# Kernel tuning notes

Hardware: AMD Instinct MI355X
Metric: run time of the kernel (lower is better)

Reference implementation:

```python
import jax, jax.numpy as jnp
import numpy as np

SCALE = 0.02  # init scale for weight matrices


def setup_inputs() -> dict:
    B, M, H = 2048, 64, 1024
    key = jax.random.key(0)
    ks = jax.random.split(key, 10)
    inp = {
        "pose_embed": jax.random.normal(ks[0], (B, H), jnp.float32),
        "query_embed": jax.random.normal(ks[1], (B, H), jnp.float32),
        "h": jax.random.normal(ks[2], (B, H), jnp.float32),
        "c": jax.random.normal(ks[3], (B, H), jnp.float32),
        "memory": jax.random.normal(ks[4], (B, M, H), jnp.float32),
        "W_ih": jax.random.normal(ks[5], (4 * H, H), jnp.float32) * SCALE,
        "W_hh": jax.random.normal(ks[6], (4 * H, H), jnp.float32) * SCALE,
        "b_ih": jnp.zeros((4 * H,), jnp.float32),
        "b_hh": jnp.zeros((4 * H,), jnp.float32),
        "Wq": jax.random.normal(ks[7], (H, H), jnp.float32) * SCALE,
        "bq": jnp.zeros((H,), jnp.float32),
        "Wk": jax.random.normal(ks[8], (H, H), jnp.float32) * SCALE,
        "bk": jnp.zeros((H,), jnp.float32),
        "Wv": jax.random.normal(ks[9], (H, H), jnp.float32) * SCALE,
        "bv": jnp.zeros((H,), jnp.float32),
    }
    return inp


def reference(pose_embed, query_embed, h, c, memory,
              W_ih, W_hh, b_ih, b_hh, Wq, bq, Wk, bk, Wv, bv):
    H = pose_embed.shape[-1]
    # --- LSTMCell step (torch gate order: i, f, g, o) ---
    gates = pose_embed @ W_ih.T + b_ih + h @ W_hh.T + b_hh  # [B, 4H]
    i_g, f_g, g_g, o_g = jnp.split(gates, 4, axis=-1)
    c_new = jax.nn.sigmoid(f_g) * c + jax.nn.sigmoid(i_g) * jnp.tanh(g_g)
    h_new = jax.nn.sigmoid(o_g) * jnp.tanh(c_new)
    # --- FIFO memory update (detach, pop oldest, append new h) ---
    mem = jnp.concatenate(
        [memory[:, 1:], jax.lax.stop_gradient(h_new)[:, None]], axis=1)  # [B, M, H]
    # --- single-query attention over memory ---
    Q = query_embed @ Wq.T + bq                       # [B, H]
    K = mem @ Wk.T + bk                               # [B, M, H]
    V = mem @ Wv.T + bv                               # [B, M, H]
    scores = jnp.einsum('bh,bmh->bm', Q, K) / jnp.sqrt(jnp.float32(H))
    attn = jax.nn.softmax(scores, axis=-1)            # [B, M]
    attended = jnp.einsum('bm,bmh->bh', attn, V)      # [B, H]
    return attended, h_new, c_new
```

## Files before the change

kernel.cpp:

```cpp
#include <hip/hip_runtime.h>
#include <stdint.h>

typedef __attribute__((ext_vector_type(8))) short short8;
typedef __attribute__((ext_vector_type(4))) float f32x4;
typedef unsigned short u16;

__device__ __forceinline__ u16 f2bf(float f) {
  union { float f; uint32_t u; } v; v.f = f;
  return (u16)((v.u + 0x7FFFu + ((v.u >> 16) & 1u)) >> 16);
}

__device__ __forceinline__ void gl_lds16(const void* g, void* l) {
  __builtin_amdgcn_global_load_lds(
      (const __attribute__((address_space(1))) void*)g,
      (__attribute__((address_space(3))) void*)l, 16, 0, 0);
}

__global__ __launch_bounds__(256) void gemm_bt(
    const u16* __restrict__ A, const u16* __restrict__ B,
    float* __restrict__ Cf, u16* __restrict__ Cb,
    const float* __restrict__ bias1,
    int M, int N, int K)
{
  __shared__ __align__(16) u16 As[128 * 32];
  __shared__ __align__(16) u16 Bs[128 * 32];
  const int t = threadIdx.x;
  const int lane = t & 63;
  const int w = t >> 6;
  const int wr = w >> 1, wc = w & 1;
  const int m0 = blockIdx.y * 128, n0 = blockIdx.x * 128;
  const int lr = lane & 15;
  const int lk = (lane >> 4) * 8;
  const int srow = t >> 2;
  const int scol = (t & 3) * 8;

  const u16* gA = A + (size_t)(m0 + srow) * K + scol;
  const u16* gB = B + (size_t)(n0 + srow) * K + scol;

  f32x4 acc[4][4] = {};

  for (int k0 = 0; k0 < K; k0 += 32) {
    gl_lds16(gA,                  As + t * 8);
    gl_lds16(gA + (size_t)64 * K, As + 2048 + t * 8);
    gl_lds16(gB,                  Bs + t * 8);
    gl_lds16(gB + (size_t)64 * K, Bs + 2048 + t * 8);
    gA += 32; gB += 32;
    __syncthreads();

    short8 a[4], b[4];
#pragma unroll
    for (int m = 0; m < 4; ++m)
      a[m] = *(const short8*)(As + (wr * 64 + m * 16 + lr) * 32 + lk);
#pragma unroll
    for (int n = 0; n < 4; ++n)
      b[n] = *(const short8*)(Bs + (wc * 64 + n * 16 + lr) * 32 + lk);
#pragma unroll
    for (int m = 0; m < 4; ++m)
#pragma unroll
      for (int n = 0; n < 4; ++n)
        acc[m][n] = __builtin_amdgcn_mfma_f32_16x16x32_bf16(a[m], b[n], acc[m][n], 0, 0, 0);
    __syncthreads();
  }

#pragma unroll
  for (int n = 0; n < 4; ++n) {
    int col = n0 + wc * 64 + n * 16 + lr;
    float bsum = bias1 ? bias1[col] : 0.f;
#pragma unroll
    for (int m = 0; m < 4; ++m) {
#pragma unroll
      for (int r = 0; r < 4; ++r) {
        int row = m0 + wr * 64 + m * 16 + (lane >> 4) * 4 + r;
        float vv = acc[m][n][r] + bsum;
        if (Cf) Cf[(size_t)row * N + col] = vv;
        if (Cb) Cb[(size_t)row * N + col] = f2bf(vv);
      }
    }
  }
}

__global__ __launch_bounds__(256) void prep_k(
    const float* __restrict__ pose, const float* __restrict__ h,
    const float* __restrict__ W_ih, const float* __restrict__ W_hh,
    const float* __restrict__ query, const float* __restrict__ Wv,
    const float* __restrict__ Wq, const float* __restrict__ Wk,
    u16* __restrict__ xcat, u16* __restrict__ wcat,
    u16* __restrict__ qry, u16* __restrict__ wvb,
    u16* __restrict__ wqb, u16* __restrict__ wktb)
{
  __shared__ u16 tile[64][65];
  int blk = blockIdx.x;
  int t = threadIdx.x;
  if (blk >= 16384) {
    int tblk = blk - 16384;
    int tr = (tblk >> 4) * 64, tc = (tblk & 15) * 64;
    int tx = t & 63;
    int ty = (t >> 6) * 16;
#pragma unroll
    for (int i = 0; i < 16; ++i)
      tile[ty + i][tx] = f2bf(Wk[(size_t)(tr + ty + i) * 1024 + tc + tx]);
    __syncthreads();
#pragma unroll
    for (int i = 0; i < 16; ++i)
      wktb[(size_t)(tc + ty + i) * 1024 + tr + tx] = tile[tx][ty + i];
    return;
  }
  const float* src; u16* dst; int ostride, ooff, base;
  if (blk < 2048)       { src = pose;  dst = xcat; ostride = 2048; ooff = 0;    base = 0; }
  else if (blk < 4096)  { src = h;     dst = xcat; ostride = 2048; ooff = 1024; base = 2048; }
  else if (blk < 8192)  { src = W_ih;  dst = wcat; ostride = 2048; ooff = 0;    base = 4096; }
  else if (blk < 12288) { src = W_hh;  dst = wcat; ostride = 2048; ooff = 1024; base = 8192; }
  else if (blk < 14336) { src = query; dst = qry;  ostride = 1024; ooff = 0;    base = 12288; }
  else if (blk < 15360) { src = Wv;    dst = wvb;  ostride = 1024; ooff = 0;    base = 14336; }
  else                  { src = Wq;    dst = wqb;  ostride = 1024; ooff = 0;    base = 15360; }
  int r = blk - base;
  int cc = t * 4;
  float4 v = *(const float4*)(src + (size_t)r * 1024 + cc);
  ushort4 o; o.x = f2bf(v.x); o.y = f2bf(v.y); o.z = f2bf(v.z); o.w = f2bf(v.w);
  *(ushort4*)(dst + (size_t)r * ostride + ooff + cc) = o;
}

__global__ __launch_bounds__(256, 3) void mega_k(
    const u16* __restrict__ Xcat, const u16* __restrict__ Wcat,
    float* __restrict__ gates,
    const float* __restrict__ b_ih, const float* __restrict__ b_hh,
    const float* __restrict__ Qk, const float* __restrict__ mem,
    float* __restrict__ attst)
{
  __shared__ __align__(16) u16 As[128 * 32];
  __shared__ __align__(16) u16 Bs[128 * 32];
  const int blk = blockIdx.x;
  const int t = threadIdx.x;
  const int lane = t & 63;

  if (blk % 3 != 2) {
    const int gid = (blk / 3) * 2 + (blk % 3);
    const int m0 = (gid >> 5) * 128, n0 = (gid & 31) * 128;
    const int w = t >> 6;
    const int wr = w >> 1, wc = w & 1;
    const int lr = lane & 15;
    const int lk = (lane >> 4) * 8;
    const int srow = t >> 2;
    const int scol = (t & 3) * 8;

    const u16* gA = Xcat + (size_t)(m0 + srow) * 2048 + scol;
    const u16* gB = Wcat + (size_t)(n0 + srow) * 2048 + scol;

    f32x4 acc[4][4] = {};
    for (int k0 = 0; k0 < 2048; k0 += 32) {
      gl_lds16(gA,                    As + t * 8);
      gl_lds16(gA + (size_t)64 * 2048, As + 2048 + t * 8);
      gl_lds16(gB,                    Bs + t * 8);
      gl_lds16(gB + (size_t)64 * 2048, Bs + 2048 + t * 8);
      gA += 32; gB += 32;
      __syncthreads();
      short8 a[4], b[4];
#pragma unroll
      for (int m = 0; m < 4; ++m)
        a[m] = *(const short8*)(As + (wr * 64 + m * 16 + lr) * 32 + lk);
#pragma unroll
      for (int n = 0; n < 4; ++n)
        b[n] = *(const short8*)(Bs + (wc * 64 + n * 16 + lr) * 32 + lk);
#pragma unroll
      for (int m = 0; m < 4; ++m)
#pragma unroll
        for (int n = 0; n < 4; ++n)
          acc[m][n] = __builtin_amdgcn_mfma_f32_16x16x32_bf16(a[m], b[n], acc[m][n], 0, 0, 0);
      __syncthreads();
    }
#pragma unroll
    for (int n = 0; n < 4; ++n) {
      int col = n0 + wc * 64 + n * 16 + lr;
      float bsum = b_ih[col] + b_hh[col];
#pragma unroll
      for (int m = 0; m < 4; ++m)
#pragma unroll
        for (int r = 0; r < 4; ++r) {
          int row = m0 + wr * 64 + m * 16 + (lane >> 4) * 4 + r;
          gates[(size_t)row * 4096 + col] = acc[m][n][r] + bsum;
        }
    }
  } else {
    const int ablk = blk / 3;
    const int wv_id = t >> 6;
    for (int bi = 0; bi < 2; ++bi) {
      const int b = ablk * 8 + wv_id * 2 + bi;
      const float* q = Qk + (size_t)b * 1024;
      float4 qv[4];
#pragma unroll
      for (int i = 0; i < 4; ++i)
        qv[i] = *(const float4*)(q + (i * 64 + lane) * 4);
      const float* mb = mem + (size_t)b * 65536;

      float m_run = -3e38f, l = 0.f;
      float4 cx[4] = {};

      for (int qd = 0; qd < 15; ++qd) {
        const float* r0 = mb + (size_t)(1 + qd * 4) * 1024;
        float4 rv[4][4];
        float s[4] = {0.f, 0.f, 0.f, 0.f};
#pragma unroll
        for (int rr = 0; rr < 4; ++rr)
#pragma unroll
          for (int i = 0; i < 4; ++i) {
            rv[rr][i] = *(const float4*)(r0 + rr * 1024 + (i * 64 + lane) * 4);
            s[rr] += rv[rr][i].x * qv[i].x + rv[rr][i].y * qv[i].y +
                     rv[rr][i].z * qv[i].z + rv[rr][i].w * qv[i].w;
          }
#pragma unroll
        for (int rr = 0; rr < 4; ++rr) {
#pragma unroll
          for (int off = 32; off; off >>= 1) s[rr] += __shfl_xor(s[rr], off);
          s[rr] *= 0.03125f;
        }
#pragma unroll
        for (int rr = 0; rr < 4; ++rr) {
          if (s[rr] <= m_run + 8.f) {
            float e = __expf(s[rr] - m_run);
            l += e;
#pragma unroll
            for (int i = 0; i < 4; ++i) {
              cx[i].x += e * rv[rr][i].x; cx[i].y += e * rv[rr][i].y;
              cx[i].z += e * rv[rr][i].z; cx[i].w += e * rv[rr][i].w;
            }
          } else {
            float sc = __expf(m_run - s[rr]);
            m_run = s[rr];
            l = l * sc + 1.f;
#pragma unroll
            for (int i = 0; i < 4; ++i) {
              cx[i].x = cx[i].x * sc + rv[rr][i].x; cx[i].y = cx[i].y * sc + rv[rr][i].y;
              cx[i].z = cx[i].z * sc + rv[rr][i].z; cx[i].w = cx[i].w * sc + rv[rr][i].w;
            }
          }
        }
      }
      for (int r = 61; r <= 63; ++r) {
        const float* row = mb + (size_t)r * 1024;
        float4 rv[4];
        float s = 0.f;
#pragma unroll
        for (int i = 0; i < 4; ++i) {
          rv[i] = *(const float4*)(row + (i * 64 + lane) * 4);
          s += rv[i].x * qv[i].x + rv[i].y * qv[i].y + rv[i].z * qv[i].z + rv[i].w * qv[i].w;
        }
#pragma unroll
        for (int off = 32; off; off >>= 1) s += __shfl_xor(s, off);
        s *= 0.03125f;
        if (s <= m_run + 8.f) {
          float e = __expf(s - m_run);
          l += e;
#pragma unroll
          for (int i = 0; i < 4; ++i) {
            cx[i].x += e * rv[i].x; cx[i].y += e * rv[i].y;
            cx[i].z += e * rv[i].z; cx[i].w += e * rv[i].w;
          }
        } else {
          float sc = __expf(m_run - s);
          m_run = s;
          l = l * sc + 1.f;
#pragma unroll
          for (int i = 0; i < 4; ++i) {
            cx[i].x = cx[i].x * sc + rv[i].x; cx[i].y = cx[i].y * sc + rv[i].y;
            cx[i].z = cx[i].z * sc + rv[i].z; cx[i].w = cx[i].w * sc + rv[i].w;
          }
        }
      }
      float* st = attst + (size_t)b * 1032;
#pragma unroll
      for (int i = 0; i < 4; ++i)
        *(float4*)(st + (i * 64 + lane) * 4) = cx[i];
      if (lane == 0) { st[1024] = m_run; st[1025] = l; }
    }
  }
}

__global__ __launch_bounds__(256) void lstmfin_k(
    const float* __restrict__ gates, const float* __restrict__ c,
    const float* __restrict__ Qk, const float* __restrict__ attst,
    float* __restrict__ out_h, float* __restrict__ out_c,
    u16* __restrict__ ctxb)
{
  const int b = blockIdx.x;
  const int t = threadIdx.x;
  const int lane = t & 63, wv_id = t >> 6;
  const int p = t * 4;
  const float* g = gates + (size_t)b * 4096;
  float4 ig = *(const float4*)(g + p);
  float4 fg = *(const float4*)(g + 1024 + p);
  float4 gg = *(const float4*)(g + 2048 + p);
  float4 og = *(const float4*)(g + 3072 + p);
  float4 cv = *(const float4*)(c + (size_t)b * 1024 + p);

  float hn[4], cn[4];
  {
    float igs[4] = {ig.x, ig.y, ig.z, ig.w};
    float fgs[4] = {fg.x, fg.y, fg.z, fg.w};
    float ggs[4] = {gg.x, gg.y, gg.z, gg.w};
    float ogs[4] = {og.x, og.y, og.z, og.w};
    float cvs[4] = {cv.x, cv.y, cv.z, cv.w};
#pragma unroll
    for (int j = 0; j < 4; ++j) {
      float si = 1.f / (1.f + __expf(-igs[j]));
      float sf = 1.f / (1.f + __expf(-fgs[j]));
      float so = 1.f / (1.f + __expf(-ogs[j]));
      float tg = 2.f / (1.f + __expf(-2.f * ggs[j])) - 1.f;
      cn[j] = sf * cvs[j] + si * tg;
      float tc2 = 2.f / (1.f + __expf(-2.f * cn[j])) - 1.f;
      hn[j] = so * tc2;
    }
  }
  *(float4*)(out_c + (size_t)b * 1024 + p) = make_float4(cn[0], cn[1], cn[2], cn[3]);
  *(float4*)(out_h + (size_t)b * 1024 + p) = make_float4(hn[0], hn[1], hn[2], hn[3]);

  float4 qv = *(const float4*)(Qk + (size_t)b * 1024 + p);
  float part = qv.x * hn[0] + qv.y * hn[1] + qv.z * hn[2] + qv.w * hn[3];
#pragma unroll
  for (int off = 32; off; off >>= 1) part += __shfl_xor(part, off);
  __shared__ float red[4];
  if (lane == 0) red[wv_id] = part;
  __syncthreads();
  float s_last = (red[0] + red[1] + red[2] + red[3]) * 0.03125f;

  const float* st = attst + (size_t)b * 1032;
  float m_run = st[1024], l = st[1025];
  float4 cx = *(const float4*)(st + p);
  if (s_last <= m_run + 8.f) {
    float e = __expf(s_last - m_run);
    l += e;
    cx.x += e * hn[0]; cx.y += e * hn[1]; cx.z += e * hn[2]; cx.w += e * hn[3];
  } else {
    float sc = __expf(m_run - s_last);
    l = l * sc + 1.f;
    cx.x = cx.x * sc + hn[0]; cx.y = cx.y * sc + hn[1];
    cx.z = cx.z * sc + hn[2]; cx.w = cx.w * sc + hn[3];
  }
  float inv = 1.f / l;
  ushort4 o;
  o.x = f2bf(cx.x * inv); o.y = f2bf(cx.y * inv);
  o.z = f2bf(cx.z * inv); o.w = f2bf(cx.w * inv);
  *(ushort4*)(ctxb + (size_t)b * 1024 + p) = o;
}

extern "C" void kernel_launch(void* const* d_in, const int* in_sizes, int n_in,
                              void* d_out, int out_size, void* d_ws, size_t ws_size,
                              hipStream_t stream) {
  const int Bb = 2048, Hh = 1024;
  const float* pose  = (const float*)d_in[0];
  const float* query = (const float*)d_in[1];
  const float* h     = (const float*)d_in[2];
  const float* c     = (const float*)d_in[3];
  const float* mem   = (const float*)d_in[4];
  const float* W_ih  = (const float*)d_in[5];
  const float* W_hh  = (const float*)d_in[6];
  const float* b_ih  = (const float*)d_in[7];
  const float* b_hh  = (const float*)d_in[8];
  const float* Wq    = (const float*)d_in[9];
  const float* bq    = (const float*)d_in[10];
  const float* Wk    = (const float*)d_in[11];
  const float* Wv    = (const float*)d_in[13];
  const float* bv    = (const float*)d_in[14];

  float* out_att = (float*)d_out;
  float* out_h   = out_att + (size_t)Bb * Hh;
  float* out_c   = out_h + (size_t)Bb * Hh;

  char* wp = (char*)d_ws;
  auto alloc = [&](size_t bytes) {
    char* p = wp; wp += (bytes + 255) & ~(size_t)255; return p;
  };
  u16*   Xcat  = (u16*)alloc((size_t)2048 * 2048 * 2);
  u16*   Wcat  = (u16*)alloc((size_t)4096 * 2048 * 2);
  u16*   Qryb  = (u16*)alloc((size_t)2048 * 1024 * 2);
  u16*   Wqb   = (u16*)alloc((size_t)1024 * 1024 * 2);
  u16*   WkTb  = (u16*)alloc((size_t)1024 * 1024 * 2);
  u16*   Qbf   = (u16*)alloc((size_t)2048 * 1024 * 2);
  u16*   Wvb   = (u16*)alloc((size_t)1024 * 1024 * 2);
  float* gates = (float*)alloc((size_t)2048 * 4096 * 4);
  float* Qk    = (float*)alloc((size_t)2048 * 1024 * 4);
  u16*   ctxb  = (u16*)alloc((size_t)2048 * 1024 * 2);
  float* attst = (float*)Qryb;

  prep_k<<<16640, 256, 0, stream>>>(pose, h, W_ih, W_hh, query, Wv, Wq, Wk,
                                    Xcat, Wcat, Qryb, Wvb, Wqb, WkTb);

  gemm_bt<<<dim3(8, 16), 256, 0, stream>>>(
      Qryb, Wqb, nullptr, Qbf, bq, 2048, 1024, 1024);

  gemm_bt<<<dim3(8, 16), 256, 0, stream>>>(
      Qbf, WkTb, Qk, nullptr, nullptr, 2048, 1024, 1024);

  mega_k<<<768, 256, 0, stream>>>(Xcat, Wcat, gates, b_ih, b_hh, Qk, mem, attst);

  lstmfin_k<<<2048, 256, 0, stream>>>(gates, c, Qk, attst, out_h, out_c, ctxb);

  gemm_bt<<<dim3(8, 16), 256, 0, stream>>>(
      ctxb, Wvb, out_att, nullptr, bv, 2048, 1024, 1024);
}
```

Before: 264.2 us.

## Precompute Wk^T·Wq product, shrink LSTM GEMM tiles, store gates in bf16

The two chained query projections (query·Wq then ·Wk) are replaced by a weight-only product G = Wk^T·Wq (1024x1024) plus a bias vector bq·Wk built with atomics. A single 2048x1024 GEMM against G then produces Qk. The gate GEMM in the fused kernel moves from 128x128 to 128x64 tiles, doubling the block count, and attention blocks handle one batch row per wave. Gates are written as bf16 to halve that buffer's traffic. The trade-off is extra rounding in the gates and in the precomputed G.

```diff
diff --git a/kernel.cpp b/kernel.cpp
--- a/kernel.cpp
+++ b/kernel.cpp
@@ -8,6 +8,9 @@
 __device__ __forceinline__ u16 f2bf(float f) {
   union { float f; uint32_t u; } v; v.f = f;
   return (u16)((v.u + 0x7FFFu + ((v.u >> 16) & 1u)) >> 16);
+}
+__device__ __forceinline__ float bf2f(u16 u) {
+  union { uint32_t u; float f; } v; v.u = (uint32_t)u << 16; return v.f;
 }
 
 __device__ __forceinline__ void gl_lds16(const void* g, void* l) {
@@ -86,23 +89,25 @@
     const float* __restrict__ Wq, const float* __restrict__ Wk,
     u16* __restrict__ xcat, u16* __restrict__ wcat,
     u16* __restrict__ qry, u16* __restrict__ wvb,
-    u16* __restrict__ wqb, u16* __restrict__ wktb)
+    u16* __restrict__ wqtb, u16* __restrict__ wktb)
 {
   __shared__ u16 tile[64][65];
   int blk = blockIdx.x;
   int t = threadIdx.x;
-  if (blk >= 16384) {
-    int tblk = blk - 16384;
+  if (blk >= 15360) {
+    const float* src; u16* dst; int tblk;
+    if (blk < 15616) { src = Wq; dst = wqtb; tblk = blk - 15360; }
+    else             { src = Wk; dst = wktb; tblk = blk - 15616; }
     int tr = (tblk >> 4) * 64, tc = (tblk & 15) * 64;
     int tx = t & 63;
     int ty = (t >> 6) * 16;
 #pragma unroll
     for (int i = 0; i < 16; ++i)
-      tile[ty + i][tx] = f2bf(Wk[(size_t)(tr + ty + i) * 1024 + tc + tx]);
+      tile[ty + i][tx] = f2bf(src[(size_t)(tr + ty + i) * 1024 + tc + tx]);
     __syncthreads();
 #pragma unroll
     for (int i = 0; i < 16; ++i)
-      wktb[(size_t)(tc + ty + i) * 1024 + tr + tx] = tile[tx][ty + i];
+      dst[(size_t)(tc + ty + i) * 1024 + tr + tx] = tile[tx][ty + i];
     return;
   }
   const float* src; u16* dst; int ostride, ooff, base;
@@ -111,8 +116,7 @@
   else if (blk < 8192)  { src = W_ih;  dst = wcat; ostride = 2048; ooff = 0;    base = 4096; }
   else if (blk < 12288) { src = W_hh;  dst = wcat; ostride = 2048; ooff = 1024; base = 8192; }
   else if (blk < 14336) { src = query; dst = qry;  ostride = 1024; ooff = 0;    base = 12288; }
-  else if (blk < 15360) { src = Wv;    dst = wvb;  ostride = 1024; ooff = 0;    base = 14336; }
-  else                  { src = Wq;    dst = wqb;  ostride = 1024; ooff = 0;    base = 15360; }
+  else                  { src = Wv;    dst = wvb;  ostride = 1024; ooff = 0;    base = 14336; }
   int r = blk - base;
   int cc = t * 4;
   float4 v = *(const float4*)(src + (size_t)r * 1024 + cc);
@@ -120,24 +124,35 @@
   *(ushort4*)(dst + (size_t)r * ostride + ooff + cc) = o;
 }
 
-__global__ __launch_bounds__(256, 3) void mega_k(
+__global__ __launch_bounds__(256) void bqwk_k(
+    const float* __restrict__ bq, const float* __restrict__ Wk,
+    float* __restrict__ qkb)
+{
+  int n = blockIdx.x * 256 + threadIdx.x;
+  int j0 = blockIdx.y * 64;
+  float s = 0.f;
+#pragma unroll 8
+  for (int j = j0; j < j0 + 64; ++j) s += bq[j] * Wk[(size_t)j * 1024 + n];
+  atomicAdd(&qkb[n], s);
+}
+
+__global__ __launch_bounds__(256, 4) void mega_k(
     const u16* __restrict__ Xcat, const u16* __restrict__ Wcat,
-    float* __restrict__ gates,
+    u16* __restrict__ gates,
     const float* __restrict__ b_ih, const float* __restrict__ b_hh,
     const float* __restrict__ Qk, const float* __restrict__ mem,
     float* __restrict__ attst)
 {
   __shared__ __align__(16) u16 As[128 * 32];
-  __shared__ __align__(16) u16 Bs[128 * 32];
+  __shared__ __align__(16) u16 Bs[64 * 32];
   const int blk = blockIdx.x;
   const int t = threadIdx.x;
   const int lane = t & 63;
 
   if (blk % 3 != 2) {
     const int gid = (blk / 3) * 2 + (blk % 3);
-    const int m0 = (gid >> 5) * 128, n0 = (gid & 31) * 128;
+    const int m0 = (gid >> 6) * 128, n0 = (gid & 63) * 64;
     const int w = t >> 6;
-    const int wr = w >> 1, wc = w & 1;
     const int lr = lane & 15;
     const int lk = (lane >> 4) * 8;
     const int srow = t >> 2;
@@ -146,23 +161,22 @@
     const u16* gA = Xcat + (size_t)(m0 + srow) * 2048 + scol;
     const u16* gB = Wcat + (size_t)(n0 + srow) * 2048 + scol;
 
-    f32x4 acc[4][4] = {};
+    f32x4 acc[2][4] = {};
     for (int k0 = 0; k0 < 2048; k0 += 32) {
-      gl_lds16(gA,                    As + t * 8);
+      gl_lds16(gA,                     As + t * 8);
       gl_lds16(gA + (size_t)64 * 2048, As + 2048 + t * 8);
-      gl_lds16(gB,                    Bs + t * 8);
-      gl_lds16(gB + (size_t)64 * 2048, Bs + 2048 + t * 8);
+      gl_lds16(gB,                     Bs + t * 8);
       gA += 32; gB += 32;
       __syncthreads();
-      short8 a[4], b[4];
-#pragma unroll
-      for (int m = 0; m < 4; ++m)
-        a[m] = *(const short8*)(As + (wr * 64 + m * 16 + lr) * 32 + lk);
+      short8 a[2], b[4];
+#pragma unroll
+      for (int m = 0; m < 2; ++m)
+        a[m] = *(const short8*)(As + (w * 32 + m * 16 + lr) * 32 + lk);
 #pragma unroll
       for (int n = 0; n < 4; ++n)
-        b[n] = *(const short8*)(Bs + (wc * 64 + n * 16 + lr) * 32 + lk);
-#pragma unroll
-      for (int m = 0; m < 4; ++m)
+        b[n] = *(const short8*)(Bs + (n * 16 + lr) * 32 + lk);
+#pragma unroll
+      for (int m = 0; m < 2; ++m)
 #pragma unroll
         for (int n = 0; n < 4; ++n)
           acc[m][n] = __builtin_amdgcn_mfma_f32_16x16x32_bf16(a[m], b[n], acc[m][n], 0, 0, 0);
@@ -170,113 +184,98 @@
     }
 #pragma unroll
     for (int n = 0; n < 4; ++n) {
-      int col = n0 + wc * 64 + n * 16 + lr;
+      int col = n0 + n * 16 + lr;
       float bsum = b_ih[col] + b_hh[col];
 #pragma unroll
-      for (int m = 0; m < 4; ++m)
+      for (int m = 0; m < 2; ++m)
 #pragma unroll
         for (int r = 0; r < 4; ++r) {
-          int row = m0 + wr * 64 + m * 16 + (lane >> 4) * 4 + r;
-          gates[(size_t)row * 4096 + col] = acc[m][n][r] + bsum;
+          int row = m0 + w * 32 + m * 16 + (lane >> 4) * 4 + r;
+          gates[(size_t)row * 4096 + col] = f2bf(acc[m][n][r] + bsum);
         }
     }
   } else {
-    const int ablk = blk / 3;
-    const int wv_id = t >> 6;
-    for (int bi = 0; bi < 2; ++bi) {
-      const int b = ablk * 8 + wv_id * 2 + bi;
-      const float* q = Qk + (size_t)b * 1024;
-      float4 qv[4];
-#pragma unroll
-      for (int i = 0; i < 4; ++i)
-        qv[i] = *(const float4*)(q + (i * 64 + lane) * 4);
-      const float* mb = mem + (size_t)b * 65536;
-
-      float m_run = -3e38f, l = 0.f;
-      float4 cx[4] = {};
-
-      for (int qd = 0; qd < 15; ++qd) {
-        const float* r0 = mb + (size_t)(1 + qd * 4) * 1024;
-        float4 rv[4][4];
-        float s[4] = {0.f, 0.f, 0.f, 0.f};
-#pragma unroll
-        for (int rr = 0; rr < 4; ++rr)
-#pragma unroll
-          for (int i = 0; i < 4; ++i) {
-            rv[rr][i] = *(const float4*)(r0 + rr * 1024 + (i * 64 + lane) * 4);
-            s[rr] += rv[rr][i].x * qv[i].x + rv[rr][i].y * qv[i].y +
-                     rv[rr][i].z * qv[i].z + rv[rr][i].w * qv[i].w;
-          }
-#pragma unroll
-        for (int rr = 0; rr < 4; ++rr) {
-#pragma unroll
-          for (int off = 32; off; off >>= 1) s[rr] += __shfl_xor(s[rr], off);
-          s[rr] *= 0.03125f;
+    const int b = (blk / 3) * 4 + (t >> 6);
+    const float* q = Qk + (size_t)b * 1024;
+    f32x4 qv[4];
+#pragma unroll
+    for (int i = 0; i < 4; ++i)
+      qv[i] = *(const f32x4*)(q + (i * 64 + lane) * 4);
+    const float* mb = mem + (size_t)b * 65536;
+
+    float m_run = -3e38f, l = 0.f;
+    f32x4 cx[4] = {};
+
+    for (int qd = 0; qd < 15; ++qd) {
+      const float* r0 = mb + (size_t)(1 + qd * 4) * 1024;
+      f32x4 rv[4][4];
+      float s[4] = {0.f, 0.f, 0.f, 0.f};
+#pragma unroll
+      for (int rr = 0; rr < 4; ++rr)
+#pragma unroll
+        for (int i = 0; i < 4; ++i) {
+          rv[rr][i] = *(const f32x4*)(r0 + rr * 1024 + (i * 64 + lane) * 4);
+          s[rr] += rv[rr][i][0] * qv[i][0] + rv[rr][i][1] * qv[i][1] +
+                   rv[rr][i][2] * qv[i][2] + rv[rr][i][3] * qv[i][3];
         }
 #pragma unroll
-        for (int rr = 0; rr < 4; ++rr) {
-          if (s[rr] <= m_run + 8.f) {
-            float e = __expf(s[rr] - m_run);
-            l += e;
-#pragma unroll
-            for (int i = 0; i < 4; ++i) {
-              cx[i].x += e * rv[rr][i].x; cx[i].y += e * rv[rr][i].y;
-              cx[i].z += e * rv[rr][i].z; cx[i].w += e * rv[rr][i].w;
-            }
-          } else {
-            float sc = __expf(m_run - s[rr]);
-            m_run = s[rr];
-            l = l * sc + 1.f;
-#pragma unroll
-            for (int i = 0; i < 4; ++i) {
-              cx[i].x = cx[i].x * sc + rv[rr][i].x; cx[i].y = cx[i].y * sc + rv[rr][i].y;
-              cx[i].z = cx[i].z * sc + rv[rr][i].z; cx[i].w = cx[i].w * sc + rv[rr][i].w;
-            }
-          }
+      for (int rr = 0; rr < 4; ++rr) {
+#pragma unroll
+        for (int off = 32; off; off >>= 1) s[rr] += __shfl_xor(s[rr], off);
+        s[rr] *= 0.03125f;
+      }
+#pragma unroll
+      for (int rr = 0; rr < 4; ++rr) {
+        if (s[rr] <= m_run + 8.f) {
+          float e = __expf(s[rr] - m_run);
+          l += e;
+#pragma unroll
+          for (int i = 0; i < 4; ++i) cx[i] += rv[rr][i] * e;
+        } else {
+          float sc = __expf(m_run - s[rr]);
+          m_run = s[rr];
+          l = l * sc + 1.f;
+#pragma unroll
+          for (int i = 0; i < 4; ++i) cx[i] = cx[i] * sc + rv[rr][i];
         }
       }
-      for (int r = 61; r <= 63; ++r) {
-        const float* row = mb + (size_t)r * 1024;
-        float4 rv[4];
-        float s = 0.f;
-#pragma unroll
-        for (int i = 0; i < 4; ++i) {
-          rv[i] = *(const float4*)(row + (i * 64 + lane) * 4);
-          s += rv[i].x * qv[i].x + rv[i].y * qv[i].y + rv[i].z * qv[i].z + rv[i].w * qv[i].w;
-        }
-#pragma unroll
-        for (int off = 32; off; off >>= 1) s += __shfl_xor(s, off);
-        s *= 0.03125f;
-        if (s <= m_run + 8.f) {
-          float e = __expf(s - m_run);
-          l += e;
-#pragma unroll
-          for (int i = 0; i < 4; ++i) {
-            cx[i].x += e * rv[i].x; cx[i].y += e * rv[i].y;
-            cx[i].z += e * rv[i].z; cx[i].w += e * rv[i].w;
-          }
-        } else {
-          float sc = __expf(m_run - s);
-          m_run = s;
-          l = l * sc + 1.f;
-#pragma unroll
-          for (int i = 0; i < 4; ++i) {
-            cx[i].x = cx[i].x * sc + rv[i].x; cx[i].y = cx[i].y * sc + rv[i].y;
-            cx[i].z = cx[i].z * sc + rv[i].z; cx[i].w = cx[i].w * sc + rv[i].w;
-          }
-        }
+    }
+    for (int r = 61; r <= 63; ++r) {
+      const float* row = mb + (size_t)r * 1024;
+      f32x4 rv[4];
+      float s = 0.f;
+#pragma unroll
+      for (int i = 0; i < 4; ++i) {
+        rv[i] = *(const f32x4*)(row + (i * 64 + lane) * 4);
+        s += rv[i][0] * qv[i][0] + rv[i][1] * qv[i][1] +
+             rv[i][2] * qv[i][2] + rv[i][3] * qv[i][3];
       }
-      float* st = attst + (size_t)b * 1032;
-#pragma unroll
-      for (int i = 0; i < 4; ++i)
-        *(float4*)(st + (i * 64 + lane) * 4) = cx[i];
-      if (lane == 0) { st[1024] = m_run; st[1025] = l; }
-    }
+#pragma unroll
+      for (int off = 32; off; off >>= 1) s += __shfl_xor(s, off);
+      s *= 0.03125f;
+      if (s <= m_run + 8.f) {
+        float e = __expf(s - m_run);
+        l += e;
+#pragma unroll
+        for (int i = 0; i < 4; ++i) cx[i] += rv[i] * e;
+      } else {
+        float sc = __expf(m_run - s);
+        m_run = s;
+        l = l * sc + 1.f;
+#pragma unroll
+        for (int i = 0; i < 4; ++i) cx[i] = cx[i] * sc + rv[i];
+      }
+    }
+    float* st = attst + (size_t)b * 1032;
+#pragma unroll
+    for (int i = 0; i < 4; ++i)
+      *(f32x4*)(st + (i * 64 + lane) * 4) = cx[i];
+    if (lane == 0) { st[1024] = m_run; st[1025] = l; }
   }
 }
 
 __global__ __launch_bounds__(256) void lstmfin_k(
-    const float* __restrict__ gates, const float* __restrict__ c,
+    const u16* __restrict__ gates, const float* __restrict__ c,
     const float* __restrict__ Qk, const float* __restrict__ attst,
     float* __restrict__ out_h, float* __restrict__ out_c,
     u16* __restrict__ ctxb)
@@ -285,19 +284,19 @@
   const int t = threadIdx.x;
   const int lane = t & 63, wv_id = t >> 6;
   const int p = t * 4;
-  const float* g = gates + (size_t)b * 4096;
-  float4 ig = *(const float4*)(g + p);
-  float4 fg = *(const float4*)(g + 1024 + p);
-  float4 gg = *(const float4*)(g + 2048 + p);
-  float4 og = *(const float4*)(g + 3072 + p);
+  const u16* g = gates + (size_t)b * 4096;
+  ushort4 igu = *(const ushort4*)(g + p);
+  ushort4 fgu = *(const ushort4*)(g + 1024 + p);
+  ushort4 ggu = *(const ushort4*)(g + 2048 + p);
+  ushort4 ogu = *(const ushort4*)(g + 3072 + p);
   float4 cv = *(const float4*)(c + (size_t)b * 1024 + p);
 
   float hn[4], cn[4];
   {
-    float igs[4] = {ig.x, ig.y, ig.z, ig.w};
-    float fgs[4] = {fg.x, fg.y, fg.z, fg.w};
-    float ggs[4] = {gg.x, gg.y, gg.z, gg.w};
-    float ogs[4] = {og.x, og.y, og.z, og.w};
+    float igs[4] = {bf2f(igu.x), bf2f(igu.y), bf2f(igu.z), bf2f(igu.w)};
+    float fgs[4] = {bf2f(fgu.x), bf2f(fgu.y), bf2f(fgu.z), bf2f(fgu.w)};
+    float ggs[4] = {bf2f(ggu.x), bf2f(ggu.y), bf2f(ggu.z), bf2f(ggu.w)};
+    float ogs[4] = {bf2f(ogu.x), bf2f(ogu.y), bf2f(ogu.z), bf2f(ogu.w)};
     float cvs[4] = {cv.x, cv.y, cv.z, cv.w};
 #pragma unroll
     for (int j = 0; j < 4; ++j) {
@@ -372,25 +371,29 @@
   u16*   Xcat  = (u16*)alloc((size_t)2048 * 2048 * 2);
   u16*   Wcat  = (u16*)alloc((size_t)4096 * 2048 * 2);
   u16*   Qryb  = (u16*)alloc((size_t)2048 * 1024 * 2);
-  u16*   Wqb   = (u16*)alloc((size_t)1024 * 1024 * 2);
+  u16*   WqTb  = (u16*)alloc((size_t)1024 * 1024 * 2);
   u16*   WkTb  = (u16*)alloc((size_t)1024 * 1024 * 2);
-  u16*   Qbf   = (u16*)alloc((size_t)2048 * 1024 * 2);
+  u16*   Gb    = (u16*)alloc((size_t)1024 * 1024 * 2);
   u16*   Wvb   = (u16*)alloc((size_t)1024 * 1024 * 2);
-  float* gates = (float*)alloc((size_t)2048 * 4096 * 4);
+  u16*   gates = (u16*)alloc((size_t)2048 * 4096 * 2);
+  float* qkb   = (float*)alloc((size_t)1024 * 4);
   float* Qk    = (float*)alloc((size_t)2048 * 1024 * 4);
   u16*   ctxb  = (u16*)alloc((size_t)2048 * 1024 * 2);
   float* attst = (float*)Qryb;
 
-  prep_k<<<16640, 256, 0, stream>>>(pose, h, W_ih, W_hh, query, Wv, Wq, Wk,
-                                    Xcat, Wcat, Qryb, Wvb, Wqb, WkTb);
+  prep_k<<<15872, 256, 0, stream>>>(pose, h, W_ih, W_hh, query, Wv, Wq, Wk,
+                                    Xcat, Wcat, Qryb, Wvb, WqTb, WkTb);
+
+  hipMemsetAsync(qkb, 0, 1024 * sizeof(float), stream);
+  bqwk_k<<<dim3(4, 16), 256, 0, stream>>>(bq, Wk, qkb);
+
+  gemm_bt<<<dim3(8, 8), 256, 0, stream>>>(
+      WkTb, WqTb, nullptr, Gb, nullptr, 1024, 1024, 1024);
 
   gemm_bt<<<dim3(8, 16), 256, 0, stream>>>(
-      Qryb, Wqb, nullptr, Qbf, bq, 2048, 1024, 1024);
-
-  gemm_bt<<<dim3(8, 16), 256, 0, stream>>>(
-      Qbf, WkTb, Qk, nullptr, nullptr, 2048, 1024, 1024);
-
-  mega_k<<<768, 256, 0, stream>>>(Xcat, Wcat, gates, b_ih, b_hh, Qk, mem, attst);
+      Qryb, Gb, Qk, nullptr, qkb, 2048, 1024, 1024);
+
+  mega_k<<<1536, 256, 0, stream>>>(Xcat, Wcat, gates, b_ih, b_hh, Qk, mem, attst);
 
   lstmfin_k<<<2048, 256, 0, stream>>>(gates, c, Qk, attst, out_h, out_c, ctxb);
 
```

Result: slower. 370.5 us (+40.2%).
